# Performance work log

Measured on AMD Instinct MI355X. Metric: run time of the kernel, lower is better.

## Reference

```python
import jax, jax.numpy as jnp
import numpy as np

N_NODES = 50000
N_EDGES = 800000
IN_C, HID_C, OUT_C = 64, 128, 64


def setup_inputs() -> dict:
    key = jax.random.key(0)
    k0, k1, k2, k3 = jax.random.split(key, 4)
    x = jax.random.normal(k0, (N_NODES, IN_C), dtype=jnp.float32)
    edge_index = jax.random.randint(k1, (2, N_EDGES), 0, N_NODES, dtype=jnp.int64)
    # Glorot-ish init for the two GCNConv linear weights
    W1 = jax.random.normal(k2, (IN_C, HID_C), dtype=jnp.float32) * (1.0 / np.sqrt(IN_C))
    b1 = jnp.zeros((HID_C,), dtype=jnp.float32)
    W2 = jax.random.normal(k3, (HID_C, OUT_C), dtype=jnp.float32) * (1.0 / np.sqrt(HID_C))
    b2 = jnp.zeros((OUT_C,), dtype=jnp.float32)
    return {"x": x, "edge_index": edge_index, "W1": W1, "b1": b1, "W2": W2, "b2": b2}


def _gcn_conv(x, src, dst, norm, W, b, n_nodes):
    # GCNConv: out = D^{-1/2} (A+I) D^{-1/2} (x W) + b
    xw = x @ W                              # [N, out_c]
    msg = xw[src] * norm[:, None]           # [E+N, out_c] gather + scale
    agg = jax.ops.segment_sum(msg, dst, num_segments=n_nodes)  # scatter-add
    return agg + b


def reference(x, edge_index, W1, b1, W2, b2):
    n = x.shape[0]
    loops = jnp.arange(n, dtype=edge_index.dtype)
    src = jnp.concatenate([edge_index[0], loops])  # add self-loops
    dst = jnp.concatenate([edge_index[1], loops])
    # symmetric normalization over A + I
    deg = jax.ops.segment_sum(jnp.ones_like(dst, dtype=x.dtype), dst, num_segments=n)
    dinv = jnp.where(deg > 0, jax.lax.rsqrt(jnp.maximum(deg, 1.0)), 0.0)
    norm = dinv[src] * dinv[dst]
    h = jax.nn.relu(_gcn_conv(x, src, dst, norm, W1, b1, n))
    return _gcn_conv(h, src, dst, norm, W2, b2, n)
```

## Files before the change

kernel.cpp:

```cpp
#include <hip/hip_runtime.h>
#include <cstdint>


#define IN_C 64
#define HID_C 128
#define OUT_C 64
#define CH 2048
#define CAP 8192

typedef short bf16x8 __attribute__((ext_vector_type(8)));
typedef float f32x4 __attribute__((ext_vector_type(4)));

__device__ __forceinline__ unsigned int f2bf(float f) {
    unsigned int u = __float_as_uint(f);
    return (u + 0x7FFFu + ((u >> 16) & 1u)) >> 16;
}
__device__ __forceinline__ float bf2f(unsigned int hi16) {
    return __uint_as_float(hi16 << 16);
}

__device__ __forceinline__ int edge_val(const void* ei, long long idx, int is64) {
    if (is64) return (int)((const long long*)ei)[idx];
    return ((const int*)ei)[idx];
}

__global__ __launch_bounds__(256) void partition_conv_k(const void* __restrict__ ei,
                                                        const float4* __restrict__ x4,
                                                        uint2* __restrict__ xbf2,
                                                        int* __restrict__ bcur,
                                                        int2* __restrict__ tmp,
                                                        int E, int NC4) {
    __shared__ int2 stage[CH];
    __shared__ int hist[256];
    __shared__ int off[256];
    __shared__ int rcur[256];
    __shared__ int goff[256];
    __shared__ int wsum[4];
    const int tid = threadIdx.x;
    const int bid = blockIdx.x;
    for (int i = bid * 256 + tid; i < NC4; i += gridDim.x * 256) {
        float4 v = x4[i];
        uint2 o;
        o.x = f2bf(v.x) | (f2bf(v.y) << 16);
        o.y = f2bf(v.z) | (f2bf(v.w) << 16);
        xbf2[i] = o;
    }
    int is64 = 1;
    {
        const unsigned int* e32 = (const unsigned int*)ei;
#pragma unroll
        for (int k = 0; k < 16; ++k) is64 &= (e32[2 * k + 1] == 0u) ? 1 : 0;
    }
    const int base = bid * CH;
    const int cnt = min(CH, E - base);
    hist[tid] = 0;
    __syncthreads();
    int sa[CH / 256], da[CH / 256];
    int ne = 0;
#pragma unroll
    for (int k = 0; k < CH / 256; ++k) {
        int i = tid + k * 256;
        if (i < cnt) {
            sa[ne] = edge_val(ei, base + i, is64);
            da[ne] = edge_val(ei, (long long)E + base + i, is64);
            ne++;
        }
    }
    for (int k = 0; k < ne; ++k) atomicAdd(&hist[da[k] >> 8], 1);
    __syncthreads();
    {
        int v = hist[tid];
        int lane = tid & 63, wid = tid >> 6;
        int s = v;
#pragma unroll
        for (int o = 1; o < 64; o <<= 1) {
            int t = __shfl_up(s, o, 64);
            if (lane >= o) s += t;
        }
        if (lane == 63) wsum[wid] = s;
        __syncthreads();
        int w = 0;
#pragma unroll
        for (int j = 0; j < 4; ++j)
            if (j < wid) w += wsum[j];
        off[tid] = w + s - v;
        rcur[tid] = w + s - v;
    }
    __syncthreads();
    for (int k = 0; k < ne; ++k) {
        int b = da[k] >> 8;
        int r = atomicAdd(&rcur[b], 1);
        stage[r] = make_int2(sa[k], da[k]);
    }
    __syncthreads();
    {
        int c = hist[tid];
        goff[tid] = tid * CAP + ((c > 0) ? atomicAdd(&bcur[tid], c) : 0);
    }
    __syncthreads();
    for (int i = tid; i < cnt; i += 256) {
        int2 e = stage[i];
        int b = e.y >> 8;
        tmp[goff[b] + (i - off[b])] = e;
    }
}

__global__ __launch_bounds__(256) void finalize_k(const int2* __restrict__ tmp,
                                                  const int* __restrict__ bcur,
                                                  int* __restrict__ rowptr,
                                                  float* __restrict__ dinv,
                                                  int* __restrict__ edata,
                                                  int N, int E) {
    __shared__ int cnt[256];
    __shared__ int cur[256];
    __shared__ int sc[256];
    __shared__ int wsum[4];
    const int tid = threadIdx.x;
    const int bid = blockIdx.x;
    const int node0 = bid << 8;
    const int lane = tid & 63, wid = tid >> 6;
    {
        int v = bcur[tid];
        int s = v;
#pragma unroll
        for (int o = 1; o < 64; o <<= 1) {
            int t = __shfl_up(s, o, 64);
            if (lane >= o) s += t;
        }
        if (lane == 63) wsum[wid] = s;
        cnt[tid] = 0;
        __syncthreads();
        int w = 0;
#pragma unroll
        for (int j = 0; j < 4; ++j)
            if (j < wid) w += wsum[j];
        sc[tid] = w + s - v;
    }
    __syncthreads();
    const int base = bid * CAP;
    const int end = base + bcur[bid];
    for (int i = base + tid; i < end; i += 256)
        atomicAdd(&cnt[tmp[i].y - node0], 1);
    __syncthreads();
    const int gi = node0 + tid;
    int v = cnt[tid];
    if (gi < N) dinv[gi] = rsqrtf((float)(v + 1));
    int s = v;
#pragma unroll
    for (int o = 1; o < 64; o <<= 1) {
        int t = __shfl_up(s, o, 64);
        if (lane >= o) s += t;
    }
    if (lane == 63) wsum[wid] = s;
    __syncthreads();
    int w = 0;
#pragma unroll
    for (int j = 0; j < 4; ++j)
        if (j < wid) w += wsum[j];
    int rp = sc[bid] + w + s - v;
    if (gi < N) rowptr[gi] = rp;
    cur[tid] = rp;
    if (bid == 0 && tid == 0) rowptr[N] = E;
    __syncthreads();
    for (int i = base + tid; i < end; i += 256) {
        int2 e = tmp[i];
        int pos = atomicAdd(&cur[e.y - node0], 1);
        edata[pos] = e.x;
    }
}

template <bool BIAS, bool OBF>
__global__ __launch_bounds__(256) void aggregate_bf16_k(const uint4* __restrict__ feat4,
                                                        const int* __restrict__ rowptr,
                                                        const int* __restrict__ edata,
                                                        const float* __restrict__ dinv,
                                                        const float4* __restrict__ bias4,
                                                        void* __restrict__ outp, int N) {
    const int tid = threadIdx.x;
    const int node = blockIdx.x * 32 + (tid >> 3);
    const int t = tid & 7;
    if (node >= N) return;
    float dn = dinv[node];
    float sl = dn * dn;
    uint4 sv = feat4[(size_t)node * 8 + t];
    float acc[8];
    acc[0] = bf2f(sv.x & 0xFFFF) * sl;
    acc[1] = bf2f(sv.x >> 16) * sl;
    acc[2] = bf2f(sv.y & 0xFFFF) * sl;
    acc[3] = bf2f(sv.y >> 16) * sl;
    acc[4] = bf2f(sv.z & 0xFFFF) * sl;
    acc[5] = bf2f(sv.z >> 16) * sl;
    acc[6] = bf2f(sv.w & 0xFFFF) * sl;
    acc[7] = bf2f(sv.w >> 16) * sl;
    int e = rowptr[node];
    const int e1 = rowptr[node + 1];
#define ACC_EDGE(V, W)                                  \
    acc[0] = fmaf((W), bf2f((V).x & 0xFFFF), acc[0]);   \
    acc[1] = fmaf((W), bf2f((V).x >> 16), acc[1]);      \
    acc[2] = fmaf((W), bf2f((V).y & 0xFFFF), acc[2]);   \
    acc[3] = fmaf((W), bf2f((V).y >> 16), acc[3]);      \
    acc[4] = fmaf((W), bf2f((V).z & 0xFFFF), acc[4]);   \
    acc[5] = fmaf((W), bf2f((V).z >> 16), acc[5]);      \
    acc[6] = fmaf((W), bf2f((V).w & 0xFFFF), acc[6]);   \
    acc[7] = fmaf((W), bf2f((V).w >> 16), acc[7]);
    for (; e + 4 <= e1; e += 4) {
        int s0 = edata[e], s1 = edata[e + 1], s2 = edata[e + 2], s3 = edata[e + 3];
        float w0 = dinv[s0] * dn, w1 = dinv[s1] * dn;
        float w2 = dinv[s2] * dn, w3 = dinv[s3] * dn;
        uint4 f0 = feat4[(size_t)s0 * 8 + t];
        uint4 f1 = feat4[(size_t)s1 * 8 + t];
        uint4 f2 = feat4[(size_t)s2 * 8 + t];
        uint4 f3 = feat4[(size_t)s3 * 8 + t];
        ACC_EDGE(f0, w0);
        ACC_EDGE(f1, w1);
        ACC_EDGE(f2, w2);
        ACC_EDGE(f3, w3);
    }
    for (; e < e1; ++e) {
        int s0 = edata[e];
        float w0 = dinv[s0] * dn;
        uint4 f0 = feat4[(size_t)s0 * 8 + t];
        ACC_EDGE(f0, w0);
    }
#undef ACC_EDGE
    if (BIAS) {
        float4 b0 = bias4[2 * t], b1v = bias4[2 * t + 1];
        acc[0] += b0.x; acc[1] += b0.y; acc[2] += b0.z; acc[3] += b0.w;
        acc[4] += b1v.x; acc[5] += b1v.y; acc[6] += b1v.z; acc[7] += b1v.w;
    }
    if (OBF) {
        uint4 o;
        o.x = f2bf(acc[0]) | (f2bf(acc[1]) << 16);
        o.y = f2bf(acc[2]) | (f2bf(acc[3]) << 16);
        o.z = f2bf(acc[4]) | (f2bf(acc[5]) << 16);
        o.w = f2bf(acc[6]) | (f2bf(acc[7]) << 16);
        ((uint4*)outp)[(size_t)node * 8 + t] = o;
    } else {
        float4* out4 = (float4*)outp;
        out4[(size_t)node * 16 + 2 * t] = make_float4(acc[0], acc[1], acc[2], acc[3]);
        out4[(size_t)node * 16 + 2 * t + 1] = make_float4(acc[4], acc[5], acc[6], acc[7]);
    }
}

__global__ __launch_bounds__(256) void gemm12_k(const uint4* __restrict__ A8,
                                                const float* __restrict__ W1,
                                                const float* __restrict__ b1,
                                                const float* __restrict__ W2,
                                                unsigned short* __restrict__ hwb, int M) {
    __shared__ uint4 As[64 * 8];
    __shared__ unsigned short B1s[128 * 64];
    __shared__ unsigned short B2s[64 * 128];
    __shared__ unsigned short Hs[64 * 128];
    const int tid = threadIdx.x;
    const int node0 = blockIdx.x * 64;
    for (int i = tid; i < 64 * 8; i += 256) {
        int r = i >> 3, c = i & 7;
        uint4 v = make_uint4(0u, 0u, 0u, 0u);
        if (node0 + r < M) v = A8[(size_t)(node0 + r) * 8 + c];
        As[r * 8 + (c ^ (r & 7))] = v;
    }
    {
        const float4* W4 = (const float4*)W1;
        for (int i = tid; i < 64 * 32; i += 256) {
            int k = i >> 5, n4 = i & 31;
            float4 v = W4[i];
            int n = n4 * 4;
#pragma unroll
            for (int j = 0; j < 4; ++j) {
                float f = (j == 0) ? v.x : (j == 1) ? v.y : (j == 2) ? v.z : v.w;
                int nn = n + j;
                int chunk = k >> 3;
                B1s[nn * 64 + (((chunk ^ (nn & 7)) << 3)) + (k & 7)] =
                    (unsigned short)f2bf(f);
            }
        }
    }
    {
        const float4* W4 = (const float4*)W2;
        for (int i = tid; i < 128 * 16; i += 256) {
            int k = i >> 4, n4 = i & 15;
            float4 v = W4[i];
            int n = n4 * 4;
#pragma unroll
            for (int j = 0; j < 4; ++j) {
                float f = (j == 0) ? v.x : (j == 1) ? v.y : (j == 2) ? v.z : v.w;
                int nn = n + j;
                int chunk = k >> 3;
                B2s[nn * 128 + ((chunk ^ (nn & 7)) << 3) + (k & 7)] =
                    (unsigned short)f2bf(f);
            }
        }
    }
    __syncthreads();

    const int lane = tid & 63;
    const int wv = tid >> 6;
    const int lr = lane & 15;
    const int lk = lane >> 4;

    {
        f32x4 acc[4][2];
#pragma unroll
        for (int mt = 0; mt < 4; ++mt)
#pragma unroll
            for (int nb = 0; nb < 2; ++nb) acc[mt][nb] = (f32x4){0.f, 0.f, 0.f, 0.f};
#pragma unroll
        for (int ks = 0; ks < 2; ++ks) {
            bf16x8 a[4], b[2];
            int chunk = ks * 4 + lk;
#pragma unroll
            for (int mt = 0; mt < 4; ++mt) {
                int r = mt * 16 + lr;
                a[mt] = __builtin_bit_cast(bf16x8, As[r * 8 + (chunk ^ (r & 7))]);
            }
#pragma unroll
            for (int nb = 0; nb < 2; ++nb) {
                int n = wv * 32 + nb * 16 + lr;
                b[nb] = __builtin_bit_cast(
                    bf16x8, ((const uint4*)(B1s + n * 64))[chunk ^ (n & 7)]);
            }
#pragma unroll
            for (int mt = 0; mt < 4; ++mt)
#pragma unroll
                for (int nb = 0; nb < 2; ++nb)
                    acc[mt][nb] = __builtin_amdgcn_mfma_f32_16x16x32_bf16(
                        a[mt], b[nb], acc[mt][nb], 0, 0, 0);
        }
#pragma unroll
        for (int nb = 0; nb < 2; ++nb) {
            int col = wv * 32 + nb * 16 + lr;
            float bb = b1[col];
            int chunk = col >> 3;
#pragma unroll
            for (int mt = 0; mt < 4; ++mt) {
#pragma unroll
                for (int j = 0; j < 4; ++j) {
                    int row = mt * 16 + lk * 4 + j;
                    float v = fmaxf(acc[mt][nb][j] + bb, 0.f);
                    Hs[row * 128 + ((chunk ^ (row & 7)) << 3) + (col & 7)] =
                        (unsigned short)f2bf(v);
                }
            }
        }
    }
    __syncthreads();

    {
        f32x4 acc[4];
#pragma unroll
        for (int mt = 0; mt < 4; ++mt) acc[mt] = (f32x4){0.f, 0.f, 0.f, 0.f};
#pragma unroll
        for (int ks = 0; ks < 4; ++ks) {
            bf16x8 a[4], b;
            int chunk = ks * 4 + lk;
#pragma unroll
            for (int mt = 0; mt < 4; ++mt) {
                int r = mt * 16 + lr;
                a[mt] = __builtin_bit_cast(
                    bf16x8, ((const uint4*)(Hs + r * 128))[chunk ^ (r & 7)]);
            }
            {
                int n = wv * 16 + lr;
                b = __builtin_bit_cast(
                    bf16x8, ((const uint4*)(B2s + n * 128))[chunk ^ (n & 7)]);
            }
#pragma unroll
            for (int mt = 0; mt < 4; ++mt)
                acc[mt] = __builtin_amdgcn_mfma_f32_16x16x32_bf16(a[mt], b, acc[mt], 0, 0, 0);
        }
        int col = wv * 16 + lr;
#pragma unroll
        for (int mt = 0; mt < 4; ++mt) {
#pragma unroll
            for (int j = 0; j < 4; ++j) {
                int row = node0 + mt * 16 + lk * 4 + j;
                if (row < M)
                    hwb[(size_t)row * OUT_C + col] = (unsigned short)f2bf(acc[mt][j]);
            }
        }
    }
}

extern "C" void kernel_launch(void* const* d_in, const int* in_sizes, int n_in,
                              void* d_out, int out_size, void* d_ws, size_t ws_size,
                              hipStream_t stream) {
    (void)n_in; (void)out_size; (void)ws_size;
    const float* x  = (const float*)d_in[0];
    const void*  ei = d_in[1];
    const float* W1 = (const float*)d_in[2];
    const float* b1 = (const float*)d_in[3];
    const float* W2 = (const float*)d_in[4];
    const float* b2 = (const float*)d_in[5];
    float* out = (float*)d_out;
    const int N = in_sizes[0] / IN_C;
    const int E = in_sizes[1] / 2;
    const int NB = (N + 255) / 256;
    const int PB = (E + CH - 1) / CH;
    const int NC4 = N * IN_C / 4;

    char* p = (char*)d_ws;
    auto take = [&](size_t bytes) {
        char* r = p;
        p += (bytes + 255) & ~(size_t)255;
        return r;
    };
    int*   rowptr  = (int*)take(((size_t)N + 1) * 4);
    float* dinv    = (float*)take((size_t)N * 4);
    int*   bcur    = (int*)take(1024);
    int*   edata   = (int*)take((size_t)E * 4);
    uint2* xbf     = (uint2*)take((size_t)N * IN_C * 2);
    uint2* hwb     = (uint2*)take((size_t)N * OUT_C * 2);
    uint2* aggA    = (uint2*)take((size_t)N * IN_C * 2);
    int2*  tmp     = (int2*)take((size_t)256 * CAP * 8);

    hipMemsetAsync(bcur, 0, 1024, stream);
    partition_conv_k<<<PB, 256, 0, stream>>>(ei, (const float4*)x, xbf, bcur, tmp, E, NC4);
    finalize_k<<<NB, 256, 0, stream>>>(tmp, bcur, rowptr, dinv, edata, N, E);

    aggregate_bf16_k<false, true><<<(N + 31) / 32, 256, 0, stream>>>(
        (const uint4*)xbf, rowptr, edata, dinv, nullptr, aggA, N);
    gemm12_k<<<(N + 63) / 64, 256, 0, stream>>>(
        (const uint4*)aggA, W1, b1, W2, (unsigned short*)hwb, N);

    aggregate_bf16_k<true, false><<<(N + 31) / 32, 256, 0, stream>>>(
        (const uint4*)hwb, rowptr, edata, dinv, (const float4*)b2, out, N);
}
```

Measured before the change: 95.12 us.

## Pack edges into 32-bit words, use 16-bit CSR indices, unroll gather by eight

Each partitioned edge is packed into one 32-bit word, with the destination in the high 16 bits and the source in the low 16, instead of an int2. The CSR source index array now uses 16-bit entries. finalize_k stages its bucket in LDS so that global tmp is read only once. The aggregate loop is unrolled to eight edges and issues all feature gathers before the dinv loads, to raise memory-level parallelism. This cuts bytes moved in the partition, finalize and aggregate passes, but it only works when node IDs fit in 16 bits (N < 65536) and it adds register pressure.

```diff
diff --git a/kernel.cpp b/kernel.cpp
--- a/kernel.cpp
+++ b/kernel.cpp
@@ -28,9 +28,9 @@
                                                         const float4* __restrict__ x4,
                                                         uint2* __restrict__ xbf2,
                                                         int* __restrict__ bcur,
-                                                        int2* __restrict__ tmp,
+                                                        unsigned int* __restrict__ tmp,
                                                         int E, int NC4) {
-    __shared__ int2 stage[CH];
+    __shared__ unsigned int stage[CH];
     __shared__ int hist[256];
     __shared__ int off[256];
     __shared__ int rcur[256];
@@ -90,7 +90,7 @@
     for (int k = 0; k < ne; ++k) {
         int b = da[k] >> 8;
         int r = atomicAdd(&rcur[b], 1);
-        stage[r] = make_int2(sa[k], da[k]);
+        stage[r] = ((unsigned int)da[k] << 16) | (unsigned int)sa[k];
     }
     __syncthreads();
     {
@@ -99,18 +99,19 @@
     }
     __syncthreads();
     for (int i = tid; i < cnt; i += 256) {
-        int2 e = stage[i];
-        int b = e.y >> 8;
+        unsigned int e = stage[i];
+        int b = e >> 24;
         tmp[goff[b] + (i - off[b])] = e;
     }
 }
 
-__global__ __launch_bounds__(256) void finalize_k(const int2* __restrict__ tmp,
+__global__ __launch_bounds__(256) void finalize_k(const unsigned int* __restrict__ tmp,
                                                   const int* __restrict__ bcur,
                                                   int* __restrict__ rowptr,
                                                   float* __restrict__ dinv,
-                                                  int* __restrict__ edata,
+                                                  unsigned short* __restrict__ edata,
                                                   int N, int E) {
+    __shared__ unsigned int stg[CAP];
     __shared__ int cnt[256];
     __shared__ int cur[256];
     __shared__ int sc[256];
@@ -138,9 +139,12 @@
     }
     __syncthreads();
     const int base = bid * CAP;
-    const int end = base + bcur[bid];
-    for (int i = base + tid; i < end; i += 256)
-        atomicAdd(&cnt[tmp[i].y - node0], 1);
+    const int bc = bcur[bid];
+    for (int i = tid; i < bc; i += 256) {
+        unsigned int e = tmp[base + i];
+        stg[i] = e;
+        atomicAdd(&cnt[(e >> 16) & 255], 1);
+    }
     __syncthreads();
     const int gi = node0 + tid;
     int v = cnt[tid];
@@ -162,17 +166,17 @@
     cur[tid] = rp;
     if (bid == 0 && tid == 0) rowptr[N] = E;
     __syncthreads();
-    for (int i = base + tid; i < end; i += 256) {
-        int2 e = tmp[i];
-        int pos = atomicAdd(&cur[e.y - node0], 1);
-        edata[pos] = e.x;
+    for (int i = tid; i < bc; i += 256) {
+        unsigned int e = stg[i];
+        int pos = atomicAdd(&cur[(e >> 16) & 255], 1);
+        edata[pos] = (unsigned short)(e & 0xFFFFu);
     }
 }
 
 template <bool BIAS, bool OBF>
 __global__ __launch_bounds__(256) void aggregate_bf16_k(const uint4* __restrict__ feat4,
                                                         const int* __restrict__ rowptr,
-                                                        const int* __restrict__ edata,
+                                                        const unsigned short* __restrict__ edata,
                                                         const float* __restrict__ dinv,
                                                         const float4* __restrict__ bias4,
                                                         void* __restrict__ outp, int N) {
@@ -203,14 +207,38 @@
     acc[5] = fmaf((W), bf2f((V).z >> 16), acc[5]);      \
     acc[6] = fmaf((W), bf2f((V).w & 0xFFFF), acc[6]);   \
     acc[7] = fmaf((W), bf2f((V).w >> 16), acc[7]);
-    for (; e + 4 <= e1; e += 4) {
+    for (; e + 8 <= e1; e += 8) {
         int s0 = edata[e], s1 = edata[e + 1], s2 = edata[e + 2], s3 = edata[e + 3];
-        float w0 = dinv[s0] * dn, w1 = dinv[s1] * dn;
-        float w2 = dinv[s2] * dn, w3 = dinv[s3] * dn;
+        int s4 = edata[e + 4], s5 = edata[e + 5], s6 = edata[e + 6], s7 = edata[e + 7];
         uint4 f0 = feat4[(size_t)s0 * 8 + t];
         uint4 f1 = feat4[(size_t)s1 * 8 + t];
         uint4 f2 = feat4[(size_t)s2 * 8 + t];
         uint4 f3 = feat4[(size_t)s3 * 8 + t];
+        uint4 f4 = feat4[(size_t)s4 * 8 + t];
+        uint4 f5 = feat4[(size_t)s5 * 8 + t];
+        uint4 f6 = feat4[(size_t)s6 * 8 + t];
+        uint4 f7 = feat4[(size_t)s7 * 8 + t];
+        float w0 = dinv[s0] * dn, w1 = dinv[s1] * dn;
+        float w2 = dinv[s2] * dn, w3 = dinv[s3] * dn;
+        float w4 = dinv[s4] * dn, w5 = dinv[s5] * dn;
+        float w6 = dinv[s6] * dn, w7 = dinv[s7] * dn;
+        ACC_EDGE(f0, w0);
+        ACC_EDGE(f1, w1);
+        ACC_EDGE(f2, w2);
+        ACC_EDGE(f3, w3);
+        ACC_EDGE(f4, w4);
+        ACC_EDGE(f5, w5);
+        ACC_EDGE(f6, w6);
+        ACC_EDGE(f7, w7);
+    }
+    for (; e + 4 <= e1; e += 4) {
+        int s0 = edata[e], s1 = edata[e + 1], s2 = edata[e + 2], s3 = edata[e + 3];
+        uint4 f0 = feat4[(size_t)s0 * 8 + t];
+        uint4 f1 = feat4[(size_t)s1 * 8 + t];
+        uint4 f2 = feat4[(size_t)s2 * 8 + t];
+        uint4 f3 = feat4[(size_t)s3 * 8 + t];
+        float w0 = dinv[s0] * dn, w1 = dinv[s1] * dn;
+        float w2 = dinv[s2] * dn, w3 = dinv[s3] * dn;
         ACC_EDGE(f0, w0);
         ACC_EDGE(f1, w1);
         ACC_EDGE(f2, w2);
@@ -404,14 +432,14 @@
         p += (bytes + 255) & ~(size_t)255;
         return r;
     };
-    int*   rowptr  = (int*)take(((size_t)N + 1) * 4);
-    float* dinv    = (float*)take((size_t)N * 4);
-    int*   bcur    = (int*)take(1024);
-    int*   edata   = (int*)take((size_t)E * 4);
-    uint2* xbf     = (uint2*)take((size_t)N * IN_C * 2);
-    uint2* hwb     = (uint2*)take((size_t)N * OUT_C * 2);
-    uint2* aggA    = (uint2*)take((size_t)N * IN_C * 2);
-    int2*  tmp     = (int2*)take((size_t)256 * CAP * 8);
+    int*            rowptr = (int*)take(((size_t)N + 1) * 4);
+    float*          dinv   = (float*)take((size_t)N * 4);
+    int*            bcur   = (int*)take(1024);
+    unsigned short* edata  = (unsigned short*)take((size_t)E * 2);
+    uint2*          xbf    = (uint2*)take((size_t)N * IN_C * 2);
+    uint2*          hwb    = (uint2*)take((size_t)N * OUT_C * 2);
+    uint2*          aggA   = (uint2*)take((size_t)N * IN_C * 2);
+    unsigned int*   tmp    = (unsigned int*)take((size_t)256 * CAP * 4);
 
     hipMemsetAsync(bcur, 0, 1024, stream);
     partition_conv_k<<<PB, 256, 0, stream>>>(ei, (const float4*)x, xbf, bcur, tmp, E, NC4);
```

After: 92.22 us. -3.1%, faster.
